# Kernel tuning notes

Measured on AMD Instinct MI355X. Metric: run time of the kernel, lower is better.

The kernel has to match this reference:

```python
import jax, jax.numpy as jnp
import numpy as np

B, L, D, H = 2, 2048, 1024, 16
Dh = D // H


def setup_inputs() -> dict:
    key = jax.random.key(0)
    ks = jax.random.split(key, 9)
    s = 1.0 / np.sqrt(D)
    inp = {
        "x": jax.random.normal(ks[0], (B, L, D), dtype=jnp.float32),
        # True above the diagonal => masked (causal)
        "causal_mask": jnp.triu(jnp.ones((L, L), dtype=bool), k=1)[None, None],
        "wq": jax.random.uniform(ks[1], (D, D), jnp.float32, -s, s),
        "bq": jax.random.uniform(ks[2], (D,), jnp.float32, -s, s),
        "wk": jax.random.uniform(ks[3], (D, D), jnp.float32, -s, s),
        "bk": jax.random.uniform(ks[4], (D,), jnp.float32, -s, s),
        "wv": jax.random.uniform(ks[5], (D, D), jnp.float32, -s, s),
        "bv": jax.random.uniform(ks[6], (D,), jnp.float32, -s, s),
        "wo": jax.random.uniform(ks[7], (D, D), jnp.float32, -s, s),
        "bo": jax.random.uniform(ks[8], (D,), jnp.float32, -s, s),
    }
    return inp


def reference(x, causal_mask, wq, bq, wk, bk, wv, bv, wo, bo):
    # projections; weights stored [in, out]-style as [D, D] used as x @ W + b
    def proj(w, b):
        return (x @ w + b).reshape(B, L, H, Dh).transpose(0, 2, 1, 3)  # [B,H,L,Dh]

    q = proj(wq, bq)
    k = proj(wk, bk)
    v = proj(wv, bv)
    scale = jnp.sqrt(jnp.asarray(Dh, x.dtype))
    scores = jnp.einsum("bhqd,bhkd->bhqk", q, k) / scale  # [B,H,L,L]
    scores = jnp.where(causal_mask[:, :, :L, :L], -jnp.inf, scores)
    attn = jax.nn.softmax(scores, axis=-1)  # dropout p=0.0 (eval)
    out = jnp.einsum("bhqk,bhkd->bhqd", attn, v)
    out = out.transpose(0, 2, 1, 3).reshape(B, L, D)
    return out @ wo + bo
```

## Files before the change

kernel.cpp:

```cpp
#include <hip/hip_runtime.h>


typedef short v8s __attribute__((ext_vector_type(8)));
typedef __bf16 v8bf __attribute__((ext_vector_type(8)));
typedef float v4f __attribute__((ext_vector_type(4)));
typedef float v16f __attribute__((ext_vector_type(16)));
typedef unsigned int uint;

#define DEV static __device__ __forceinline__

DEV short f2bf(float f) {
  unsigned u = __builtin_bit_cast(unsigned, f);
  u += 0x7FFFu + ((u >> 16) & 1u);
  return (short)(u >> 16);
}

DEV uint pack2(float lo, float hi) {
  return (uint)(unsigned short)f2bf(lo) | ((uint)(unsigned short)f2bf(hi) << 16);
}

DEV v4f mfma16(v8s a, v8s b, v4f c) {
  return __builtin_amdgcn_mfma_f32_16x16x32_bf16(
      __builtin_bit_cast(v8bf, a), __builtin_bit_cast(v8bf, b), c, 0, 0, 0);
}

DEV v16f mfma32(v8s a, v8s b, v16f c) {
  return __builtin_amdgcn_mfma_f32_32x32x16_bf16(
      __builtin_bit_cast(v8bf, a), __builtin_bit_cast(v8bf, b), c, 0, 0, 0);
}

#define GLDS16(g, l)                                                         \
  __builtin_amdgcn_global_load_lds(                                          \
      (__attribute__((address_space(1))) void*)(g),                          \
      (__attribute__((address_space(3))) void*)(l), 16, 0, 0)

__global__ __launch_bounds__(256) void k_cvt(const float* __restrict__ x,
                                             short* __restrict__ xb) {
  int i = blockIdx.x * 256 + threadIdx.x;
  float4 v = reinterpret_cast<const float4*>(x)[i];
  short4 o;
  o.x = f2bf(v.x); o.y = f2bf(v.y); o.z = f2bf(v.z); o.w = f2bf(v.w);
  reinterpret_cast<short4*>(xb)[i] = o;
}

__global__ __launch_bounds__(256) void k_tw(const float* __restrict__ wq,
                                            const float* __restrict__ wk,
                                            const float* __restrict__ wv,
                                            const float* __restrict__ wo,
                                            short* __restrict__ wqkvT,
                                            short* __restrict__ woT) {
  __shared__ float t[32][33];
  int wi = blockIdx.z;
  const float* src = (wi == 0) ? wq : (wi == 1) ? wk : (wi == 2) ? wv : wo;
  short* dst = (wi < 3) ? (wqkvT + wi * 1024 * 1024) : woT;
  int n0 = blockIdx.x * 32, k0 = blockIdx.y * 32;
  int tx = threadIdx.x, ty = threadIdx.y;
#pragma unroll
  for (int i = 0; i < 4; i++)
    t[ty + i * 8][tx] = src[(k0 + ty + i * 8) * 1024 + n0 + tx];
  __syncthreads();
#pragma unroll
  for (int i = 0; i < 4; i++)
    dst[(n0 + ty + i * 8) * 1024 + k0 + tx] = f2bf(t[tx][ty + i * 8]);
}

template <int MODE>
__global__ __launch_bounds__(256) void k_gemm(
    const short* __restrict__ A, const short* __restrict__ BT,
    const float* __restrict__ b0, const float* __restrict__ b1,
    const float* __restrict__ b2, short* __restrict__ Qo,
    short* __restrict__ Ko, short* __restrict__ VTo,
    float* __restrict__ outF) {
  constexpr int K = 1024;
  __shared__ short As[128 * 64], Bs[128 * 64];
  __shared__ short SL[64 * 132];
  const int tid = threadIdx.x;
  const int w = tid >> 6, lane = tid & 63;
  const int wr = w >> 1, wc = w & 1;
  const int bm = blockIdx.y, bn = blockIdx.x;
  const int lr = lane & 15, lg = lane >> 4;

  const int rA = tid >> 3;
  const int cbs = ((tid & 7) * 16) ^ ((rA & 7) << 4);
  const short* pA[4];
  const short* pB[4];
#pragma unroll
  for (int i = 0; i < 4; i++) {
    pA[i] = A + (size_t)(bm * 128 + rA + i * 32) * K + (cbs >> 1);
    pB[i] = BT + (size_t)(bn * 128 + rA + i * 32) * K + (cbs >> 1);
  }

  v4f acc[4][4] = {};
  for (int kt = 0; kt < K / 64; ++kt) {
#pragma unroll
    for (int i = 0; i < 4; i++) {
      GLDS16(pA[i] + kt * 64, As + i * 2048 + w * 512);
      GLDS16(pB[i] + kt * 64, Bs + i * 2048 + w * 512);
    }
    __syncthreads();
#pragma unroll
    for (int ks = 0; ks < 2; ++ks) {
      v8s af[4], bf[4];
#pragma unroll
      for (int mf = 0; mf < 4; mf++) {
        int R = wr * 64 + mf * 16 + lr;
        int byo = (R * 128 + ks * 64 + lg * 16) ^ ((R & 7) << 4);
        af[mf] = *reinterpret_cast<const v8s*>(
            reinterpret_cast<const char*>(As) + byo);
      }
#pragma unroll
      for (int nf = 0; nf < 4; nf++) {
        int R = wc * 64 + nf * 16 + lr;
        int byo = (R * 128 + ks * 64 + lg * 16) ^ ((R & 7) << 4);
        bf[nf] = *reinterpret_cast<const v8s*>(
            reinterpret_cast<const char*>(Bs) + byo);
      }
      __builtin_amdgcn_s_setprio(1);
#pragma unroll
      for (int mf = 0; mf < 4; mf++)
#pragma unroll
        for (int nf = 0; nf < 4; nf++)
          acc[mf][nf] = mfma16(af[mf], bf[nf], acc[mf][nf]);
      __builtin_amdgcn_s_setprio(0);
    }
    __syncthreads();
  }

  if constexpr (MODE == 0) {
    if (bn < 16) {
#pragma unroll
      for (int mf = 0; mf < 4; mf++) {
#pragma unroll
        for (int nf = 0; nf < 4; nf++) {
#pragma unroll
          for (int r = 0; r < 4; r++) {
            int mrow = bm * 128 + wr * 64 + mf * 16 + lg * 4 + r;
            int ncol = bn * 128 + wc * 64 + nf * 16 + lr;
            int which = ncol >> 10, d = ncol & 1023;
            float v = acc[mf][nf][r] + ((which == 0) ? b0[d] : b1[d]);
            int h = d >> 6, dh = d & 63;
            int bb = mrow >> 11, lp = mrow & 2047;
            if (which == 0)
              Qo[((size_t)(bb * 16 + h) * 2048 + lp) * 64 + dh] =
                  f2bf(v * 0.18033688011112043f);
            else
              Ko[((size_t)(bb * 16 + h) * 2048 + lp) * 64 + dh] = f2bf(v);
          }
        }
      }
    } else {
      const int bb = bm >> 4;
      const int lp0 = (bm & 15) * 128;
#pragma unroll
      for (int hh = 0; hh < 2; ++hh) {
        if (wc == hh) {
#pragma unroll
          for (int mf = 0; mf < 4; mf++)
#pragma unroll
            for (int nf = 0; nf < 4; nf++)
#pragma unroll
              for (int r = 0; r < 4; r++) {
                int mrow_l = wr * 64 + mf * 16 + lg * 4 + r;
                int ncol_l = nf * 16 + lr;
                int d = (bn - 16) * 128 + hh * 64 + ncol_l;
                SL[ncol_l * 132 + mrow_l] = f2bf(acc[mf][nf][r] + b2[d]);
              }
        }
        __syncthreads();
        int h = (bn - 16) * 2 + hh;
        int row = tid >> 2;
#pragma unroll
        for (int q = 0; q < 4; q++) {
          int col = ((tid & 3) + q * 4) * 8;
          *reinterpret_cast<v8s*>(
              VTo + ((size_t)(bb * 16 + h) * 64 + row) * 2048 + lp0 + col) =
              *reinterpret_cast<const v8s*>(SL + row * 132 + col);
        }
        __syncthreads();
      }
    }
  } else {
#pragma unroll
    for (int mf = 0; mf < 4; mf++)
#pragma unroll
      for (int nf = 0; nf < 4; nf++)
#pragma unroll
        for (int r = 0; r < 4; r++) {
          int mrow = bm * 128 + wr * 64 + mf * 16 + lg * 4 + r;
          int ncol = bn * 128 + wc * 64 + nf * 16 + lr;
          outF[(size_t)mrow * 1024 + ncol] = acc[mf][nf][r] + b0[ncol];
        }
  }
}

__global__ __launch_bounds__(256) void k_flash(const short* __restrict__ Qg,
                                               const short* __restrict__ Kg,
                                               const short* __restrict__ VTg,
                                               short* __restrict__ ctx) {
  __shared__ short Kl[2][64 * 64], Vl[2][64 * 64];
  const int tid = threadIdx.x, w = tid >> 6, lane = tid & 63;
  const int l31 = lane & 31, hi = lane >> 5;
  const int y = blockIdx.y;
  const int bh = y;
  const int qt = (y < 16) ? (15 - (int)blockIdx.x) : (int)blockIdx.x;
  const int q = qt * 128 + w * 32 + l31;

  v8s qf[4];
  {
    const short* qrow = Qg + ((size_t)bh * 2048 + q) * 64 + hi * 8;
#pragma unroll
    for (int dc = 0; dc < 4; dc++)
      qf[dc] = *reinterpret_cast<const v8s*>(qrow + dc * 16);
  }

  float m = -1e30f, l = 0.f;
  v16f o0 = {}, o1 = {};

  const int rA = tid >> 3;
  const int cs8 = ((tid & 7) ^ (rA & 7)) * 8;
  const short* kb = Kg + (size_t)bh * 2048 * 64;
  const short* vb = VTg + (size_t)bh * 64 * 2048;

  const int nt = 2 * qt + 2;
  int c = 0;
#define STAGE(kt_, cc_)                                                       \
  {                                                                           \
    _Pragma("unroll") for (int i = 0; i < 2; i++) {                           \
      GLDS16(kb + (size_t)((kt_)*64 + rA + i * 32) * 64 + cs8,                \
             &Kl[cc_][i * 2048 + w * 512]);                                   \
      GLDS16(vb + (size_t)(rA + i * 32) * 2048 + (kt_)*64 + cs8,              \
             &Vl[cc_][i * 2048 + w * 512]);                                   \
    }                                                                         \
  }
  STAGE(0, 0);

  const int rxor = (l31 & 7) << 4;
  const int rowb = l31 * 128;

  for (int kt = 0; kt < nt; ++kt) {
    __syncthreads();
    if (kt + 1 < nt) STAGE(kt + 1, c ^ 1);

    v16f s0 = {}, s1 = {};
    const char* Klc = reinterpret_cast<const char*>(Kl[c]);
    __builtin_amdgcn_s_setprio(1);
#pragma unroll
    for (int dc = 0; dc < 4; dc++) {
      int cb = (dc * 32 + hi * 16) ^ rxor;
      v8s k0 = *reinterpret_cast<const v8s*>(Klc + rowb + cb);
      v8s k1 = *reinterpret_cast<const v8s*>(Klc + 4096 + rowb + cb);
      s0 = mfma32(k0, qf[dc], s0);
      s1 = mfma32(k1, qf[dc], s1);
    }
    __builtin_amdgcn_s_setprio(0);

    if (kt >= 2 * qt) {
      int kb0 = kt * 64 + 4 * hi;
#pragma unroll
      for (int r = 0; r < 16; r++) {
        int kv = kb0 + (r & 3) + 8 * (r >> 2);
        if (kv > q) s0[r] = -1e30f;
        if (kv + 32 > q) s1[r] = -1e30f;
      }
    }

    float pm = s0[0];
#pragma unroll
    for (int r = 1; r < 16; r++) pm = fmaxf(pm, s0[r]);
#pragma unroll
    for (int r = 0; r < 16; r++) pm = fmaxf(pm, s1[r]);
    pm = fmaxf(pm, __shfl_xor(pm, 32, 64));
    if (__any(pm - m > 8.0f)) {
      float mn = fmaxf(m, pm);
      float alpha = exp2f(m - mn);
      m = mn;
      l *= alpha;
#pragma unroll
      for (int r = 0; r < 16; r++) { o0[r] *= alpha; o1[r] *= alpha; }
    }
    float rs = 0.f;
#pragma unroll
    for (int r = 0; r < 16; r++) {
      s0[r] = exp2f(fminf(s0[r] - m, 126.0f));
      rs += s0[r];
    }
#pragma unroll
    for (int r = 0; r < 16; r++) {
      s1[r] = exp2f(fminf(s1[r] - m, 126.0f));
      rs += s1[r];
    }
    l += rs + __shfl_xor(rs, 32, 64);

    uint W0[8], W1[8];
#pragma unroll
    for (int t = 0; t < 8; t++) {
      W0[t] = pack2(s0[2 * t], s0[2 * t + 1]);
      W1[t] = pack2(s1[2 * t], s1[2 * t + 1]);
    }

    const char* Vlc = reinterpret_cast<const char*>(Vl[c]);
#pragma unroll
    for (int kc = 0; kc < 4; kc++) {
      uint S0, S1, S2, S3;
      if (kc == 0) { S0 = W0[0]; S1 = W0[1]; S2 = W0[2]; S3 = W0[3]; }
      else if (kc == 1) { S0 = W0[4]; S1 = W0[5]; S2 = W0[6]; S3 = W0[7]; }
      else if (kc == 2) { S0 = W1[0]; S1 = W1[1]; S2 = W1[2]; S3 = W1[3]; }
      else { S0 = W1[4]; S1 = W1[5]; S2 = W1[6]; S3 = W1[7]; }
      uint x0 = __shfl_xor(hi ? S0 : S2, 32, 64);
      uint x1 = __shfl_xor(hi ? S1 : S3, 32, 64);
      uint u0 = hi ? x0 : S0;
      uint u1 = hi ? x1 : S1;
      uint u2 = hi ? S2 : x0;
      uint u3 = hi ? S3 : x1;
      uint4 uf = {u0, u1, u2, u3};
      v8s pf = __builtin_bit_cast(v8s, uf);
      int cb = (kc * 32 + hi * 16) ^ rxor;
      v8s v0 = *reinterpret_cast<const v8s*>(Vlc + rowb + cb);
      v8s v1 = *reinterpret_cast<const v8s*>(Vlc + 4096 + rowb + cb);
      __builtin_amdgcn_s_setprio(1);
      o0 = mfma32(v0, pf, o0);
      o1 = mfma32(v1, pf, o1);
      __builtin_amdgcn_s_setprio(0);
    }
    c ^= 1;
  }

  const int h = bh & 15, bb = bh >> 4;
  float inv = 1.0f / l;
  short* orow = ctx + ((size_t)(bb * 2048 + q)) * 1024 + h * 64;
#pragma unroll
  for (int df = 0; df < 2; df++) {
#pragma unroll
    for (int g = 0; g < 4; g++) {
      short4 st;
      const v16f& o = df ? o1 : o0;
      st.x = f2bf(o[g * 4 + 0] * inv);
      st.y = f2bf(o[g * 4 + 1] * inv);
      st.z = f2bf(o[g * 4 + 2] * inv);
      st.w = f2bf(o[g * 4 + 3] * inv);
      *reinterpret_cast<short4*>(orow + df * 32 + 8 * g + 4 * hi) = st;
    }
  }
}

extern "C" void kernel_launch(void* const* d_in, const int* in_sizes, int n_in,
                              void* d_out, int out_size, void* d_ws,
                              size_t ws_size, hipStream_t stream) {
  (void)in_sizes; (void)n_in; (void)out_size; (void)ws_size;
  const float* x = (const float*)d_in[0];
  const float* wq = (const float*)d_in[2];
  const float* bq = (const float*)d_in[3];
  const float* wk = (const float*)d_in[4];
  const float* bk = (const float*)d_in[5];
  const float* wv = (const float*)d_in[6];
  const float* bv = (const float*)d_in[7];
  const float* wo = (const float*)d_in[8];
  const float* bo = (const float*)d_in[9];

  char* ws = (char*)d_ws;
  short* xb = (short*)(ws);
  short* wqkvT = (short*)(ws + (8u << 20));
  short* woT = (short*)(ws + (14u << 20));
  short* Qb = (short*)(ws + (16u << 20));
  short* Kb = (short*)(ws + (24u << 20));
  short* VTb = (short*)(ws + (32u << 20));
  short* ctx = xb;
  float* out = (float*)d_out;

  k_cvt<<<4096, 256, 0, stream>>>(x, xb);
  k_tw<<<dim3(32, 32, 4), dim3(32, 8), 0, stream>>>(wq, wk, wv, wo, wqkvT, woT);
  k_gemm<0><<<dim3(24, 32), 256, 0, stream>>>(xb, wqkvT, bq, bk, bv, Qb, Kb,
                                              VTb, nullptr);
  k_flash<<<dim3(16, 32), 256, 0, stream>>>(Qb, Kb, VTb, ctx);
  k_gemm<1><<<dim3(8, 32), 256, 0, stream>>>(ctx, woT, bo, nullptr, nullptr,
                                             nullptr, nullptr, nullptr, out);
}
```

Before: 232.7 us.

## Use 128-wide KV tiles in flash attention and reorder block scheduling

Doubles the key/value tile processed per iteration from 64 to 128, which halves the loop trip count, halves the barriers per query tile and raises MFMA work between syncs. The LDS staging layout and swizzle change to match, and the grid is transposed so blockIdx.x indexes batch-head, with query-tile ordering paired so heavy and light causal tiles interleave. It also switches to the raw hardware exp2 intrinsic without clamping. The cost is more LDS (64KB double-buffered) and more registers for four score accumulators, which may lower occupancy, and the diagonal tile now wastes more masked compute.

```diff
diff --git a/kernel.cpp b/kernel.cpp
--- a/kernel.cpp
+++ b/kernel.cpp
@@ -197,12 +197,13 @@
                                                const short* __restrict__ Kg,
                                                const short* __restrict__ VTg,
                                                short* __restrict__ ctx) {
-  __shared__ short Kl[2][64 * 64], Vl[2][64 * 64];
+  __shared__ short Kl[2][128 * 64];
+  __shared__ short Vl[2][64 * 128];
   const int tid = threadIdx.x, w = tid >> 6, lane = tid & 63;
   const int l31 = lane & 31, hi = lane >> 5;
+  const int bh = blockIdx.x;
   const int y = blockIdx.y;
-  const int bh = y;
-  const int qt = (y < 16) ? (15 - (int)blockIdx.x) : (int)blockIdx.x;
+  const int qt = (y < 8) ? y : 23 - y;
   const int q = qt * 128 + w * 32 + l31;
 
   v8s qf[4];
@@ -216,51 +217,63 @@
   float m = -1e30f, l = 0.f;
   v16f o0 = {}, o1 = {};
 
-  const int rA = tid >> 3;
-  const int cs8 = ((tid & 7) ^ (rA & 7)) * 8;
   const short* kb = Kg + (size_t)bh * 2048 * 64;
   const short* vb = VTg + (size_t)bh * 64 * 2048;
 
-  const int nt = 2 * qt + 2;
+  const int lKr = lane >> 3;
+  const int lKc = ((lane & 7) ^ lKr) * 8;
+  const int lVr = lane >> 4;
+  const int w4 = w * 4;
+
+  const int nt = qt + 1;
   int c = 0;
-#define STAGE(kt_, cc_)                                                       \
-  {                                                                           \
-    _Pragma("unroll") for (int i = 0; i < 2; i++) {                           \
-      GLDS16(kb + (size_t)((kt_)*64 + rA + i * 32) * 64 + cs8,                \
-             &Kl[cc_][i * 2048 + w * 512]);                                   \
-      GLDS16(vb + (size_t)(rA + i * 32) * 2048 + (kt_)*64 + cs8,              \
-             &Vl[cc_][i * 2048 + w * 512]);                                   \
-    }                                                                         \
+#define STAGE(kt_, cc_)                                                        \
+  {                                                                            \
+    _Pragma("unroll") for (int i = 0; i < 4; i++) {                            \
+      int ii = w4 + i;                                                         \
+      GLDS16(kb + (size_t)((kt_)*128 + ii * 8 + lKr) * 64 + lKc,               \
+             &Kl[cc_][ii * 512]);                                              \
+      int vr = ii * 4 + lVr;                                                   \
+      GLDS16(vb + (size_t)vr * 2048 + (kt_)*128 + ((lane & 15) ^ (vr & 7)) * 8,\
+             &Vl[cc_][ii * 512]);                                              \
+    }                                                                          \
   }
   STAGE(0, 0);
 
-  const int rxor = (l31 & 7) << 4;
-  const int rowb = l31 * 128;
+  const int rx = (l31 & 7) << 4;
+  const int krb = l31 * 128;
+  const int vrb = l31 * 256;
 
   for (int kt = 0; kt < nt; ++kt) {
     __syncthreads();
     if (kt + 1 < nt) STAGE(kt + 1, c ^ 1);
 
-    v16f s0 = {}, s1 = {};
+    v16f s0 = {}, s1 = {}, s2 = {}, s3 = {};
     const char* Klc = reinterpret_cast<const char*>(Kl[c]);
     __builtin_amdgcn_s_setprio(1);
 #pragma unroll
     for (int dc = 0; dc < 4; dc++) {
-      int cb = (dc * 32 + hi * 16) ^ rxor;
-      v8s k0 = *reinterpret_cast<const v8s*>(Klc + rowb + cb);
-      v8s k1 = *reinterpret_cast<const v8s*>(Klc + 4096 + rowb + cb);
+      int cb = (dc * 32 + hi * 16) ^ rx;
+      v8s k0 = *reinterpret_cast<const v8s*>(Klc + krb + cb);
+      v8s k1 = *reinterpret_cast<const v8s*>(Klc + 4096 + krb + cb);
+      v8s k2 = *reinterpret_cast<const v8s*>(Klc + 8192 + krb + cb);
+      v8s k3 = *reinterpret_cast<const v8s*>(Klc + 12288 + krb + cb);
       s0 = mfma32(k0, qf[dc], s0);
       s1 = mfma32(k1, qf[dc], s1);
+      s2 = mfma32(k2, qf[dc], s2);
+      s3 = mfma32(k3, qf[dc], s3);
     }
     __builtin_amdgcn_s_setprio(0);
 
-    if (kt >= 2 * qt) {
-      int kb0 = kt * 64 + 4 * hi;
+    if (kt == qt) {
+      int kb0 = kt * 128 + 4 * hi;
 #pragma unroll
       for (int r = 0; r < 16; r++) {
         int kv = kb0 + (r & 3) + 8 * (r >> 2);
         if (kv > q) s0[r] = -1e30f;
         if (kv + 32 > q) s1[r] = -1e30f;
+        if (kv + 64 > q) s2[r] = -1e30f;
+        if (kv + 96 > q) s3[r] = -1e30f;
       }
     }
 
@@ -269,10 +282,14 @@
     for (int r = 1; r < 16; r++) pm = fmaxf(pm, s0[r]);
 #pragma unroll
     for (int r = 0; r < 16; r++) pm = fmaxf(pm, s1[r]);
+#pragma unroll
+    for (int r = 0; r < 16; r++) pm = fmaxf(pm, s2[r]);
+#pragma unroll
+    for (int r = 0; r < 16; r++) pm = fmaxf(pm, s3[r]);
     pm = fmaxf(pm, __shfl_xor(pm, 32, 64));
     if (__any(pm - m > 8.0f)) {
       float mn = fmaxf(m, pm);
-      float alpha = exp2f(m - mn);
+      float alpha = __builtin_amdgcn_exp2f(m - mn);
       m = mn;
       l *= alpha;
 #pragma unroll
@@ -281,47 +298,54 @@
     float rs = 0.f;
 #pragma unroll
     for (int r = 0; r < 16; r++) {
-      s0[r] = exp2f(fminf(s0[r] - m, 126.0f));
-      rs += s0[r];
+      s0[r] = __builtin_amdgcn_exp2f(s0[r] - m); rs += s0[r];
     }
 #pragma unroll
     for (int r = 0; r < 16; r++) {
-      s1[r] = exp2f(fminf(s1[r] - m, 126.0f));
-      rs += s1[r];
+      s1[r] = __builtin_amdgcn_exp2f(s1[r] - m); rs += s1[r];
+    }
+#pragma unroll
+    for (int r = 0; r < 16; r++) {
+      s2[r] = __builtin_amdgcn_exp2f(s2[r] - m); rs += s2[r];
+    }
+#pragma unroll
+    for (int r = 0; r < 16; r++) {
+      s3[r] = __builtin_amdgcn_exp2f(s3[r] - m); rs += s3[r];
     }
     l += rs + __shfl_xor(rs, 32, 64);
 
-    uint W0[8], W1[8];
+    uint W0[8], W1[8], W2[8], W3[8];
 #pragma unroll
     for (int t = 0; t < 8; t++) {
       W0[t] = pack2(s0[2 * t], s0[2 * t + 1]);
       W1[t] = pack2(s1[2 * t], s1[2 * t + 1]);
+      W2[t] = pack2(s2[2 * t], s2[2 * t + 1]);
+      W3[t] = pack2(s3[2 * t], s3[2 * t + 1]);
     }
 
     const char* Vlc = reinterpret_cast<const char*>(Vl[c]);
-#pragma unroll
-    for (int kc = 0; kc < 4; kc++) {
-      uint S0, S1, S2, S3;
-      if (kc == 0) { S0 = W0[0]; S1 = W0[1]; S2 = W0[2]; S3 = W0[3]; }
-      else if (kc == 1) { S0 = W0[4]; S1 = W0[5]; S2 = W0[6]; S3 = W0[7]; }
-      else if (kc == 2) { S0 = W1[0]; S1 = W1[1]; S2 = W1[2]; S3 = W1[3]; }
-      else { S0 = W1[4]; S1 = W1[5]; S2 = W1[6]; S3 = W1[7]; }
+    __builtin_amdgcn_s_setprio(1);
+#pragma unroll
+    for (int kc = 0; kc < 8; kc++) {
+      const uint* Wp = (kc < 2) ? W0 : (kc < 4) ? W1 : (kc < 6) ? W2 : W3;
+      int base = (kc & 1) * 4;
+      uint S0 = Wp[base + 0], S1 = Wp[base + 1];
+      uint S2 = Wp[base + 2], S3 = Wp[base + 3];
       uint x0 = __shfl_xor(hi ? S0 : S2, 32, 64);
       uint x1 = __shfl_xor(hi ? S1 : S3, 32, 64);
-      uint u0 = hi ? x0 : S0;
-      uint u1 = hi ? x1 : S1;
-      uint u2 = hi ? S2 : x0;
-      uint u3 = hi ? S3 : x1;
-      uint4 uf = {u0, u1, u2, u3};
+      uint4 uf;
+      uf.x = hi ? x0 : S0;
+      uf.y = hi ? x1 : S1;
+      uf.z = hi ? S2 : x0;
+      uf.w = hi ? S3 : x1;
       v8s pf = __builtin_bit_cast(v8s, uf);
-      int cb = (kc * 32 + hi * 16) ^ rxor;
-      v8s v0 = *reinterpret_cast<const v8s*>(Vlc + rowb + cb);
-      v8s v1 = *reinterpret_cast<const v8s*>(Vlc + 4096 + rowb + cb);
-      __builtin_amdgcn_s_setprio(1);
+      int cb = (kc * 32 + hi * 16) ^ rx;
+      v8s v0 = *reinterpret_cast<const v8s*>(Vlc + vrb + cb);
+      v8s v1 = *reinterpret_cast<const v8s*>(Vlc + 8192 + vrb + cb);
       o0 = mfma32(v0, pf, o0);
       o1 = mfma32(v1, pf, o1);
-      __builtin_amdgcn_s_setprio(0);
-    }
+    }
+    __builtin_amdgcn_s_setprio(0);
     c ^= 1;
   }
 
@@ -371,7 +395,7 @@
   k_tw<<<dim3(32, 32, 4), dim3(32, 8), 0, stream>>>(wq, wk, wv, wo, wqkvT, woT);
   k_gemm<0><<<dim3(24, 32), 256, 0, stream>>>(xb, wqkvT, bq, bk, bv, Qb, Kb,
                                               VTb, nullptr);
-  k_flash<<<dim3(16, 32), 256, 0, stream>>>(Qb, Kb, VTb, ctx);
+  k_flash<<<dim3(32, 16), 256, 0, stream>>>(Qb, Kb, VTb, ctx);
   k_gemm<1><<<dim3(8, 32), 256, 0, stream>>>(ctx, woT, bo, nullptr, nullptr,
                                              nullptr, nullptr, nullptr, out);
 }
```

Result: faster. 212.7 us (-8.6%).
